# Kernel optimization log

Hardware: AMD Instinct MI355X
Metric: run time of the kernel (lower is better)

## Reference

```python
import jax, jax.numpy as jnp
import numpy as np

B, N, C_IN, C_OUT, K = 2, 8192, 128, 128, 21  # K = num_neighbors + 1 (self)
EPS = 1e-5

def knn_idx(xyz, k):
    # xyz: [B,N,3] -> idx [B,N,k] of k nearest neighbors (self included)
    d2 = jnp.sum(xyz * xyz, axis=-1)  # [B,N]
    dist = d2[:, :, None] + d2[:, None, :] - 2.0 * jnp.einsum('bnd,bmd->bnm', xyz, xyz)
    _, idx = jax.lax.top_k(-dist, k)
    return idx

def group_points(pts, idx):
    # pts [B,N,D], idx [B,N,K] -> [B,N,K,D]
    return jax.vmap(lambda p, i: p[i])(pts, idx)

def group_feats(f, idx):
    # f [B,C,N], idx [B,N,K] -> [B,C,N,K]
    return jax.vmap(lambda ff, i: ff[:, i])(f, idx)

def conv_bn_relu(x, W, g, b, m, v):
    # 1x1 conv (bias=False) + BatchNorm (inference stats) + ReLU
    y = jnp.einsum('oc,bcnk->bonk', W, x)
    inv = g / jnp.sqrt(v + EPS)
    return jax.nn.relu(y * inv[None, :, None, None] + (b - m * inv)[None, :, None, None])

def setup_inputs():
    key = jax.random.key(0)
    ks = jax.random.split(key, 12)
    return {
        'xyz': jax.random.normal(ks[0], (B, N, 3), jnp.float32),
        'f': jax.random.normal(ks[1], (B, C_IN, N), jnp.float32),
        'W_geo': jax.random.normal(ks[2], (C_OUT, 6), jnp.float32) * 0.1,
        'g_geo': jax.random.uniform(ks[3], (C_OUT,), jnp.float32, 0.5, 1.5),
        'b_geo': jax.random.normal(ks[4], (C_OUT,), jnp.float32) * 0.1,
        'm_geo': jax.random.normal(ks[5], (C_OUT,), jnp.float32) * 0.1,
        'v_geo': jax.random.uniform(ks[6], (C_OUT,), jnp.float32, 0.5, 1.5),
        'W_feat': jax.random.normal(ks[7], (C_OUT, 2 * C_IN), jnp.float32) * 0.05,
        'g_feat': jax.random.uniform(ks[8], (C_OUT,), jnp.float32, 0.5, 1.5),
        'b_feat': jax.random.normal(ks[9], (C_OUT,), jnp.float32) * 0.1,
        'm_feat': jax.random.normal(ks[10], (C_OUT,), jnp.float32) * 0.1,
        'v_feat': jax.random.uniform(ks[11], (C_OUT,), jnp.float32, 0.5, 1.5),
    }

def reference(xyz, f, W_geo, g_geo, b_geo, m_geo, v_geo, W_feat, g_feat, b_feat, m_feat, v_feat):
    idx = knn_idx(xyz, K)                                   # [B,N,K]
    grouped_xyz = group_points(xyz, idx)                    # [B,N,K,3]
    xyz_diff = jnp.transpose(grouped_xyz - xyz[:, :, None, :], (0, 3, 1, 2))  # [B,3,N,K]
    center = jnp.broadcast_to(jnp.transpose(xyz, (0, 2, 1))[:, :, :, None], (B, 3, N, K))
    G_geo = jnp.concatenate([center, xyz_diff], axis=1)     # [B,6,N,K]
    grouped_f = group_feats(f, idx)                         # [B,C,N,K]
    center_f = jnp.broadcast_to(f[:, :, :, None], (B, C_IN, N, K))
    G_feat = jnp.concatenate([center_f, grouped_f - center_f], axis=1)  # [B,2C,N,K]
    G_geo = conv_bn_relu(G_geo, W_geo, g_geo, b_geo, m_geo, v_geo)      # [B,C_OUT,N,K]
    G_feat = conv_bn_relu(G_feat, W_feat, g_feat, b_feat, m_feat, v_feat)
    feature = jnp.concatenate([G_geo, G_feat], axis=1)      # [B,2*C_OUT,N,K]
    return jnp.max(feature, axis=-1)                        # [B,2*C_OUT,N]
```

## Files before the change

kernel.cpp:

```cpp
#include <hip/hip_runtime.h>

typedef unsigned int u32;
typedef unsigned long long u64;
typedef unsigned short u16;
typedef float v2f __attribute__((ext_vector_type(2)));

#define DEV __device__ __forceinline__

DEV u16 f2bf(float x) {
  u32 u = __float_as_uint(x);
  u32 r = u + 0x7fffu + ((u >> 16) & 1u);
  return (u16)(r >> 16);
}
DEV float bflo(u32 d) { return __uint_as_float(d << 16); }
DEV float bfhi(u32 d) { return __uint_as_float(d & 0xffff0000u); }
DEV u64 sortable64(double f) {
  long long b = __double_as_longlong(f);
  return (u64)b ^ (u64)((b >> 63) | (long long)0x8000000000000000ll);
}
DEV double ddist(double qx, double qy, double qz, double qd2,
                 float mxf, float myf, float mzf) {
  double cx = (double)mxf, cy = (double)myf, cz = (double)mzf;
  double cd2 = cx * cx + cy * cy + cz * cz;
  double dot = cx * qx + cy * qy + cz * qz;
  return (qd2 + cd2) - 2.0 * dot;
}
DEV float fmin3f(float a, float b, float c) {
  return __builtin_fminf(__builtin_fminf(a, b), c);
}
DEV v2f vfma2(v2f a, v2f b, v2f c) { return __builtin_elementwise_fma(a, b, c); }

#define NB 2
#define NN 8192
#define NC 128
#define KK 21
#define MARGIN 1e-3f
#define CT 2048

__global__ __launch_bounds__(256) void k_prep(
    const float* __restrict__ Wf, const float* __restrict__ gf, const float* __restrict__ bf_,
    const float* __restrict__ mf, const float* __restrict__ vf,
    const float* __restrict__ Wg, const float* __restrict__ gg, const float* __restrict__ bg,
    const float* __restrict__ mg, const float* __restrict__ vg,
    u16* __restrict__ Wt, float* __restrict__ beta_f,
    float* __restrict__ Wgu, float* __restrict__ Wgv, float* __restrict__ beta_g) {
  int g = blockIdx.x * 256 + threadIdx.x;
  int c = g >> 8, o = g & 255;
  float val;
  if (o < 128) {
    float inv = gf[o] / sqrtf(vf[o] + 1e-5f);
    val = inv * (Wf[o * 256 + c] - Wf[o * 256 + c + 128]);
  } else {
    int o2 = o - 128;
    float inv = gf[o2] / sqrtf(vf[o2] + 1e-5f);
    val = inv * Wf[o2 * 256 + c + 128];
  }
  Wt[c * 256 + o] = f2bf(val);
  if (g < 128) {
    float inv = gf[g] / sqrtf(vf[g] + 1e-5f);
    beta_f[g] = bf_[g] - mf[g] * inv;
  } else if (g < 256) {
    int oo = g - 128;
    float invg = gg[oo] / sqrtf(vg[oo] + 1e-5f);
#pragma unroll
    for (int d = 0; d < 3; ++d) {
      Wgu[oo * 3 + d] = invg * (Wg[oo * 6 + d] - Wg[oo * 6 + 3 + d]);
      Wgv[oo * 3 + d] = invg * Wg[oo * 6 + 3 + d];
    }
    beta_g[oo] = bg[oo] - mg[oo] * invg;
  }
}

__global__ __launch_bounds__(256) void k_geo(
    const float* __restrict__ xyz, const float* __restrict__ Wgu, const float* __restrict__ Wgv,
    const float* __restrict__ beta_g, u32* __restrict__ ucat, u32* __restrict__ vcat) {
  int g = blockIdx.x * 256 + threadIdx.x;
  int p = g >> 6, oc = g & 63;
  const float* xp = xyz + p * 3;
  float X = xp[0], Y = xp[1], Z = xp[2];
  u32 du = 0, dv = 0;
#pragma unroll
  for (int h = 0; h < 2; ++h) {
    int o = oc * 2 + h;
    float ug = X * Wgu[o * 3] + Y * Wgu[o * 3 + 1] + Z * Wgu[o * 3 + 2] + beta_g[o];
    float vv = X * Wgv[o * 3] + Y * Wgv[o * 3 + 1] + Z * Wgv[o * 3 + 2];
    du |= (u32)f2bf(ug) << (16 * h);
    dv |= (u32)f2bf(vv) << (16 * h);
  }
  ucat[p * 128 + oc] = du;
  vcat[p * 128 + oc] = dv;
}

__global__ __launch_bounds__(256) void k_feat(
    const float* __restrict__ f, const u32* __restrict__ Wt32, const float* __restrict__ beta_f,
    u32* __restrict__ ucat, u32* __restrict__ vcat) {
  __shared__ u32 sW[128 * 128];
  __shared__ float sF[128][68];

  const int t = threadIdx.x;
  const int b = blockIdx.x >> 7;
  const int n0 = (blockIdx.x & 127) << 6;
  const int boff = b * (NC * NN);

#pragma unroll
  for (int k = 0; k < 64; ++k) sW[t + (k << 8)] = Wt32[t + (k << 8)];
#pragma unroll
  for (int k = 0; k < 32; ++k) {
    int i = t + (k << 8);
    int c = i >> 6, col = i & 63;
    sF[c][col] = f[boff + c * NN + n0 + col];
  }
  __syncthreads();

  const int w = t >> 6, lane = t & 63;
  const int og = lane >> 3, pg = lane & 7;
  const int o0 = w * 64 + og * 8;
  const int p0 = pg * 8;

  float acc[8][8];
#pragma unroll
  for (int a = 0; a < 8; ++a)
#pragma unroll
    for (int p = 0; p < 8; ++p) acc[a][p] = 0.0f;

  for (int c = 0; c < 128; ++c) {
    float4 fa = *(const float4*)&sF[c][p0];
    float4 fb = *(const float4*)&sF[c][p0 + 4];
    uint4 wr = *(const uint4*)&sW[c * 128 + (o0 >> 1)];
    float wv[8] = {bflo(wr.x), bfhi(wr.x), bflo(wr.y), bfhi(wr.y),
                   bflo(wr.z), bfhi(wr.z), bflo(wr.w), bfhi(wr.w)};
    float fv[8] = {fa.x, fa.y, fa.z, fa.w, fb.x, fb.y, fb.z, fb.w};
#pragma unroll
    for (int a = 0; a < 8; ++a)
#pragma unroll
      for (int p = 0; p < 8; ++p) acc[a][p] = __builtin_fmaf(wv[a], fv[p], acc[a][p]);
  }

  const int ochan = o0 & 127;
  const bool is_u = (o0 < 128);
  float bet[8];
#pragma unroll
  for (int a = 0; a < 8; ++a) bet[a] = is_u ? beta_f[ochan + a] : 0.0f;
  u32* dstbase = is_u ? ucat : vcat;
#pragma unroll
  for (int p = 0; p < 8; ++p) {
    int pt = (b << 13) + n0 + p0 + p;
    u32 d0 = (u32)f2bf(acc[0][p] + bet[0]) | ((u32)f2bf(acc[1][p] + bet[1]) << 16);
    u32 d1 = (u32)f2bf(acc[2][p] + bet[2]) | ((u32)f2bf(acc[3][p] + bet[3]) << 16);
    u32 d2 = (u32)f2bf(acc[4][p] + bet[4]) | ((u32)f2bf(acc[5][p] + bet[5]) << 16);
    u32 d3 = (u32)f2bf(acc[6][p] + bet[6]) | ((u32)f2bf(acc[7][p] + bet[7]) << 16);
    *(uint4*)&dstbase[pt * 128 + 64 + (ochan >> 1)] = make_uint4(d0, d1, d2, d3);
  }
}

__global__ __launch_bounds__(256, 4) void k_knn(const float* __restrict__ xyz,
                                                int* __restrict__ knn) {
  __shared__ float sx[CT], sy[CT], sz[CT];
  __shared__ u16 ssurv[16][128];
  __shared__ u32 scnt[16];
  __shared__ float sthr[2][16];

  const int t = threadIdx.x;
  const int blk = blockIdx.x;
  const int b = blk >> 9;
  const int n0 = (blk & 511) << 4;
  const float* X = xyz + b * (NN * 3);

  if (t < 16) scnt[t] = 0u;

  const int w = t >> 6, lane = t & 63;
  const int g = w >> 1;
  const int h = w & 1;
  const int hb = h << 10;

  float mx[8], my[8], mz[8];
#pragma unroll
  for (int i = 0; i < 8; ++i) {
    int q = n0 + (g << 3) + i;
    mx[i] = -2.0f * X[q * 3];
    my[i] = -2.0f * X[q * 3 + 1];
    mz[i] = -2.0f * X[q * 3 + 2];
  }

  float mn[8];
#pragma unroll
  for (int i = 0; i < 8; ++i) mn[i] = __builtin_inff();

  for (int ct = 0; ct < NN / CT; ++ct) {
    __syncthreads();
    const float* Xt = X + ct * (CT * 3);
#pragma unroll
    for (int g2 = 0; g2 < 2; ++g2) {
      int c0 = (t << 2) + (g2 << 10);
      const float* src = Xt + c0 * 3;
      float4 q0 = *(const float4*)(src);
      float4 q1 = *(const float4*)(src + 4);
      float4 q2 = *(const float4*)(src + 8);
      *(float4*)&sx[c0] = make_float4(q0.x, q0.w, q1.z, q2.y);
      *(float4*)&sy[c0] = make_float4(q0.y, q1.x, q1.w, q2.z);
      *(float4*)&sz[c0] = make_float4(q0.z, q1.y, q2.x, q2.w);
    }
    __syncthreads();
#pragma unroll 2
    for (int s8 = 0; s8 < 4; ++s8) {
      int cb = hb + (s8 << 8) + (lane << 2);
      float4 X4 = *(const float4*)&sx[cb];
      float4 Y4 = *(const float4*)&sy[cb];
      float4 Z4 = *(const float4*)&sz[cb];
      v2f x01 = {X4.x, X4.y}, x23 = {X4.z, X4.w};
      v2f y01 = {Y4.x, Y4.y}, y23 = {Y4.z, Y4.w};
      v2f z01 = {Z4.x, Z4.y}, z23 = {Z4.z, Z4.w};
      v2f w01 = vfma2(x01, x01, vfma2(y01, y01, z01 * z01));
      v2f w23 = vfma2(x23, x23, vfma2(y23, y23, z23 * z23));
#pragma unroll
      for (int i = 0; i < 8; ++i) {
        v2f mxv = {mx[i], mx[i]}, myv = {my[i], my[i]}, mzv = {mz[i], mz[i]};
        v2f s01 = vfma2(x01, mxv, vfma2(y01, myv, vfma2(z01, mzv, w01)));
        v2f s23 = vfma2(x23, mxv, vfma2(y23, myv, vfma2(z23, mzv, w23)));
        mn[i] = fmin3f(mn[i], s01.x, s01.y);
        mn[i] = fmin3f(mn[i], s23.x, s23.y);
      }
    }
  }

#pragma unroll 1
  for (int i = 0; i < 8; ++i) {
    float v = mn[i];
#pragma unroll
    for (int k = 2; k <= 64; k <<= 1) {
#pragma unroll
      for (int j = k >> 1; j > 0; j >>= 1) {
        float p = __shfl_xor(v, j);
        bool takeMin = (((lane & k) == 0) == ((lane & j) == 0));
        v = takeMin ? fminf(v, p) : fmaxf(v, p);
      }
    }
    float tw = __shfl(v, 20);
    if (lane == 0) sthr[h][(g << 3) + i] = tw;
  }
  __syncthreads();
  float thr[8];
#pragma unroll
  for (int i = 0; i < 8; ++i) {
    int qq = (g << 3) + i;
    thr[i] = fminf(sthr[0][qq], sthr[1][qq]) + MARGIN;
  }

  for (int ct = 0; ct < NN / CT; ++ct) {
    __syncthreads();
    const float* Xt = X + ct * (CT * 3);
#pragma unroll
    for (int g2 = 0; g2 < 2; ++g2) {
      int c0 = (t << 2) + (g2 << 10);
      const float* src = Xt + c0 * 3;
      float4 q0 = *(const float4*)(src);
      float4 q1 = *(const float4*)(src + 4);
      float4 q2 = *(const float4*)(src + 8);
      *(float4*)&sx[c0] = make_float4(q0.x, q0.w, q1.z, q2.y);
      *(float4*)&sy[c0] = make_float4(q0.y, q1.x, q1.w, q2.z);
      *(float4*)&sz[c0] = make_float4(q0.z, q1.y, q2.x, q2.w);
    }
    __syncthreads();
#pragma unroll 1
    for (int s8 = 0; s8 < 4; ++s8) {
      int cb = hb + (s8 << 8) + (lane << 2);
      float4 X4 = *(const float4*)&sx[cb];
      float4 Y4 = *(const float4*)&sy[cb];
      float4 Z4 = *(const float4*)&sz[cb];
      v2f x01 = {X4.x, X4.y}, x23 = {X4.z, X4.w};
      v2f y01 = {Y4.x, Y4.y}, y23 = {Y4.z, Y4.w};
      v2f z01 = {Z4.x, Z4.y}, z23 = {Z4.z, Z4.w};
      v2f w01 = vfma2(x01, x01, vfma2(y01, y01, z01 * z01));
      v2f w23 = vfma2(x23, x23, vfma2(y23, y23, z23 * z23));
      int mbase = ct * CT + cb;
#pragma unroll
      for (int i = 0; i < 8; ++i) {
        v2f mxv = {mx[i], mx[i]}, myv = {my[i], my[i]}, mzv = {mz[i], mz[i]};
        v2f s01 = vfma2(x01, mxv, vfma2(y01, myv, vfma2(z01, mzv, w01)));
        v2f s23 = vfma2(x23, mxv, vfma2(y23, myv, vfma2(z23, mzv, w23)));
        int qq = (g << 3) + i;
        if (s01.x <= thr[i]) {
          u32 slot = atomicAdd(&scnt[qq], 1u);
          if (slot < 128u) ssurv[qq][slot] = (u16)(mbase + 0);
        }
        if (s01.y <= thr[i]) {
          u32 slot = atomicAdd(&scnt[qq], 1u);
          if (slot < 128u) ssurv[qq][slot] = (u16)(mbase + 1);
        }
        if (s23.x <= thr[i]) {
          u32 slot = atomicAdd(&scnt[qq], 1u);
          if (slot < 128u) ssurv[qq][slot] = (u16)(mbase + 2);
        }
        if (s23.y <= thr[i]) {
          u32 slot = atomicAdd(&scnt[qq], 1u);
          if (slot < 128u) ssurv[qq][slot] = (u16)(mbase + 3);
        }
      }
    }
  }
  __syncthreads();

#pragma unroll 1
  for (int i = 0; i < 4; ++i) {
    const int qq = (w << 2) + i;
    const int q = n0 + qq;
    double Qx = (double)X[q * 3], Qy = (double)X[q * 3 + 1], Qz = (double)X[q * 3 + 2];
    double Qd2 = Qx * Qx + Qy * Qy + Qz * Qz;
    u32 cnt = scnt[qq];
    if (cnt > 128u) cnt = 128u;
    int* outp = knn + ((b << 13) + q) * KK;

    bool v0 = ((u32)lane < cnt);
    u32 m0 = v0 ? (u32)ssurv[qq][lane] : 0u;
    double s0 = ddist(Qx, Qy, Qz, Qd2, X[m0 * 3], X[m0 * 3 + 1], X[m0 * 3 + 2]);
    u64 k0 = v0 ? ((sortable64(s0) & 0xFFFFFFFFFFFFE000ull) | (u64)m0) : ~0ull;

    if (cnt <= 64u) {
      u64 v = k0;
#pragma unroll
      for (int k = 2; k <= 64; k <<= 1) {
#pragma unroll
        for (int j = k >> 1; j > 0; j >>= 1) {
          u64 p = __shfl_xor(v, j);
          bool takeMin = (((lane & k) == 0) == ((lane & j) == 0));
          bool pl = p < v;
          u64 mnv = pl ? p : v;
          u64 mxv = pl ? v : p;
          v = takeMin ? mnv : mxv;
        }
      }
      if (lane < KK) outp[lane] = (int)(v & 8191ull);
    } else {
      bool v1 = ((u32)(lane + 64) < cnt);
      u32 m1 = v1 ? (u32)ssurv[qq][lane + 64] : 0u;
      double s1 = ddist(Qx, Qy, Qz, Qd2, X[m1 * 3], X[m1 * 3 + 1], X[m1 * 3 + 2]);
      u64 k1 = v1 ? ((sortable64(s1) & 0xFFFFFFFFFFFFE000ull) | (u64)m1) : ~0ull;
      u32 selm = 0;
      for (int r = 0; r < KK; ++r) {
        u64 mk = (k0 < k1) ? k0 : k1;
#pragma unroll
        for (int j = 32; j > 0; j >>= 1) {
          u64 p = __shfl_xor(mk, j);
          if (p < mk) mk = p;
        }
        if (k0 == mk) k0 = ~0ull;
        else if (k1 == mk) k1 = ~0ull;
        if (lane == r) selm = (u32)(mk & 8191ull);
      }
      if (lane < KK) outp[lane] = (int)selm;
    }
  }
}

__global__ __launch_bounds__(256) void k_gather(
    const u32* __restrict__ ucat, const u32* __restrict__ vcat,
    const int* __restrict__ knn, float* __restrict__ out) {
  __shared__ float tr[64 * 258];

  const int t = threadIdx.x;
  const int b = blockIdx.x >> 7;
  const int n0 = (blockIdx.x & 127) << 6;
  const int w = t >> 6, lane = t & 63;
  const int which = w >> 1;
  const int lo = ((w & 1) << 6) | lane;

  for (int step = 0; step < 32; ++step) {
    int qq = step * 2 + which;
    int q = n0 + qq;
    const int* ip = knn + ((b << 13) + q) * KK;
    float a0 = -__builtin_inff(), a1 = -__builtin_inff();
#pragma unroll
    for (int k = 0; k < KK; ++k) {
      int p = ip[k];
      u32 d = vcat[(((b << 13) + p) << 7) + lo];
      a0 = fmaxf(a0, bflo(d));
      a1 = fmaxf(a1, bfhi(d));
    }
    u32 u = ucat[(((b << 13) + q) << 7) + lo];
    float r0 = fmaxf(bflo(u) + a0, 0.0f);
    float r1 = fmaxf(bfhi(u) + a1, 0.0f);
    *(float2*)&tr[qq * 258 + 2 * lo] = make_float2(r0, r1);
  }
  __syncthreads();

  float* ob = out + b * (256 * NN);
  for (int i = 0; i < 64; ++i) {
    int o = (w << 6) + i;
    ob[o * NN + n0 + lane] = tr[lane * 258 + o];
  }
}

extern "C" void kernel_launch(void* const* d_in, const int* in_sizes, int n_in,
                              void* d_out, int out_size, void* d_ws, size_t ws_size,
                              hipStream_t stream) {
  const float* xyz = (const float*)d_in[0];
  const float* f   = (const float*)d_in[1];
  const float* Wg  = (const float*)d_in[2];
  const float* gg  = (const float*)d_in[3];
  const float* bg  = (const float*)d_in[4];
  const float* mg  = (const float*)d_in[5];
  const float* vg  = (const float*)d_in[6];
  const float* Wf  = (const float*)d_in[7];
  const float* gf  = (const float*)d_in[8];
  const float* bf_ = (const float*)d_in[9];
  const float* mf  = (const float*)d_in[10];
  const float* vf  = (const float*)d_in[11];

  char* ws = (char*)d_ws;
  u16*   Wt     = (u16*)ws;
  float* beta_f = (float*)(ws + 65536);
  float* Wgu    = (float*)(ws + 66048);
  float* Wgv    = (float*)(ws + 67584);
  float* beta_g = (float*)(ws + 69120);
  u32*   ucat   = (u32*)(ws + 69632);
  u32*   vcat   = (u32*)(ws + 69632 + 8388608);
  int*   knn    = (int*)(ws + 69632 + 2 * 8388608);
  float* out    = (float*)d_out;

  if (ws_size < (size_t)(69632 + 2 * 8388608 + 16384 * KK * 4)) return;

  k_prep<<<dim3(128), dim3(256), 0, stream>>>(Wf, gf, bf_, mf, vf, Wg, gg, bg, mg, vg,
                                              Wt, beta_f, Wgu, Wgv, beta_g);
  k_geo<<<dim3(4096), dim3(256), 0, stream>>>(xyz, Wgu, Wgv, beta_g, ucat, vcat);
  k_feat<<<dim3(256), dim3(256), 0, stream>>>(f, (const u32*)Wt, beta_f, ucat, vcat);
  k_knn<<<dim3(1024), dim3(256), 0, stream>>>(xyz, knn);
  k_gather<<<dim3(256), dim3(256), 0, stream>>>(ucat, vcat, knn, out);
}
```

Baseline: 200.3 us.

## Restructure kNN blocks to 8 queries with 4-wave candidate split and precomputed norms

The kNN kernel now gives each block 8 queries instead of 16, doubling the grid, and each of the four waves scans a quarter of every 1024-point candidate tile. Candidate squared norms are computed once per tile and stored in shared memory, and the per-wave thresholds are reduced across four waves. The filter pass tests the minimum of four distances first, so most candidates skip the per-candidate atomic checks. Launch bounds go to 8 blocks per SM, which raises occupancy, but each block now rereads all of xyz for half as many queries and runs twice as many tile barriers.

```diff
diff --git a/kernel.cpp b/kernel.cpp
--- a/kernel.cpp
+++ b/kernel.cpp
@@ -35,7 +35,6 @@
 #define NC 128
 #define KK 21
 #define MARGIN 1e-3f
-#define CT 2048
 
 __global__ __launch_bounds__(256) void k_prep(
     const float* __restrict__ Wf, const float* __restrict__ gf, const float* __restrict__ bf_,
@@ -153,73 +152,68 @@
   }
 }
 
-__global__ __launch_bounds__(256, 4) void k_knn(const float* __restrict__ xyz,
+__global__ __launch_bounds__(256, 8) void k_knn(const float* __restrict__ xyz,
                                                 int* __restrict__ knn) {
-  __shared__ float sx[CT], sy[CT], sz[CT];
-  __shared__ u16 ssurv[16][128];
-  __shared__ u32 scnt[16];
-  __shared__ float sthr[2][16];
+  __shared__ float sx[1024], sy[1024], sz[1024], sd[1024];
+  __shared__ u16 ssurv[8][128];
+  __shared__ u32 scnt[8];
+  __shared__ float sthr[4][8];
 
   const int t = threadIdx.x;
   const int blk = blockIdx.x;
-  const int b = blk >> 9;
-  const int n0 = (blk & 511) << 4;
+  const int b = blk >> 10;
+  const int n0 = (blk & 1023) << 3;
   const float* X = xyz + b * (NN * 3);
 
-  if (t < 16) scnt[t] = 0u;
+  if (t < 8) scnt[t] = 0u;
 
   const int w = t >> 6, lane = t & 63;
-  const int g = w >> 1;
-  const int h = w & 1;
-  const int hb = h << 10;
-
-  float mx[8], my[8], mz[8];
+  const int ci = (w << 8) + (lane << 2);
+
+  float mx[8], my[8], mz[8], mn[8];
 #pragma unroll
   for (int i = 0; i < 8; ++i) {
-    int q = n0 + (g << 3) + i;
+    int q = n0 + i;
     mx[i] = -2.0f * X[q * 3];
     my[i] = -2.0f * X[q * 3 + 1];
     mz[i] = -2.0f * X[q * 3 + 2];
-  }
-
-  float mn[8];
-#pragma unroll
-  for (int i = 0; i < 8; ++i) mn[i] = __builtin_inff();
-
-  for (int ct = 0; ct < NN / CT; ++ct) {
+    mn[i] = __builtin_inff();
+  }
+
+  for (int ct = 0; ct < 8; ++ct) {
     __syncthreads();
-    const float* Xt = X + ct * (CT * 3);
-#pragma unroll
-    for (int g2 = 0; g2 < 2; ++g2) {
-      int c0 = (t << 2) + (g2 << 10);
-      const float* src = Xt + c0 * 3;
+    {
+      const float* src = X + ct * 3072 + t * 12;
       float4 q0 = *(const float4*)(src);
       float4 q1 = *(const float4*)(src + 4);
       float4 q2 = *(const float4*)(src + 8);
+      int c0 = t << 2;
       *(float4*)&sx[c0] = make_float4(q0.x, q0.w, q1.z, q2.y);
       *(float4*)&sy[c0] = make_float4(q0.y, q1.x, q1.w, q2.z);
       *(float4*)&sz[c0] = make_float4(q0.z, q1.y, q2.x, q2.w);
-    }
-    __syncthreads();
-#pragma unroll 2
-    for (int s8 = 0; s8 < 4; ++s8) {
-      int cb = hb + (s8 << 8) + (lane << 2);
-      float4 X4 = *(const float4*)&sx[cb];
-      float4 Y4 = *(const float4*)&sy[cb];
-      float4 Z4 = *(const float4*)&sz[cb];
-      v2f x01 = {X4.x, X4.y}, x23 = {X4.z, X4.w};
-      v2f y01 = {Y4.x, Y4.y}, y23 = {Y4.z, Y4.w};
-      v2f z01 = {Z4.x, Z4.y}, z23 = {Z4.z, Z4.w};
+      v2f x01 = {q0.x, q0.w}, x23 = {q1.z, q2.y};
+      v2f y01 = {q0.y, q1.x}, y23 = {q1.w, q2.z};
+      v2f z01 = {q0.z, q1.y}, z23 = {q2.x, q2.w};
       v2f w01 = vfma2(x01, x01, vfma2(y01, y01, z01 * z01));
       v2f w23 = vfma2(x23, x23, vfma2(y23, y23, z23 * z23));
-#pragma unroll
-      for (int i = 0; i < 8; ++i) {
-        v2f mxv = {mx[i], mx[i]}, myv = {my[i], my[i]}, mzv = {mz[i], mz[i]};
-        v2f s01 = vfma2(x01, mxv, vfma2(y01, myv, vfma2(z01, mzv, w01)));
-        v2f s23 = vfma2(x23, mxv, vfma2(y23, myv, vfma2(z23, mzv, w23)));
-        mn[i] = fmin3f(mn[i], s01.x, s01.y);
-        mn[i] = fmin3f(mn[i], s23.x, s23.y);
-      }
+      *(float4*)&sd[c0] = make_float4(w01.x, w01.y, w23.x, w23.y);
+    }
+    __syncthreads();
+    float4 X4 = *(const float4*)&sx[ci];
+    float4 Y4 = *(const float4*)&sy[ci];
+    float4 Z4 = *(const float4*)&sz[ci];
+    float4 D4 = *(const float4*)&sd[ci];
+    v2f x01 = {X4.x, X4.y}, x23 = {X4.z, X4.w};
+    v2f y01 = {Y4.x, Y4.y}, y23 = {Y4.z, Y4.w};
+    v2f z01 = {Z4.x, Z4.y}, z23 = {Z4.z, Z4.w};
+    v2f w01 = {D4.x, D4.y}, w23 = {D4.z, D4.w};
+#pragma unroll
+    for (int i = 0; i < 8; ++i) {
+      v2f mxv = {mx[i], mx[i]}, myv = {my[i], my[i]}, mzv = {mz[i], mz[i]};
+      v2f s01 = vfma2(x01, mxv, vfma2(y01, myv, vfma2(z01, mzv, w01)));
+      v2f s23 = vfma2(x23, mxv, vfma2(y23, myv, vfma2(z23, mzv, w23)));
+      mn[i] = fmin3f(mn[i], s01.x, s01.y);
+      mn[i] = fmin3f(mn[i], s23.x, s23.y);
     }
   }
 
@@ -236,64 +230,65 @@
       }
     }
     float tw = __shfl(v, 20);
-    if (lane == 0) sthr[h][(g << 3) + i] = tw;
+    if (lane == 0) sthr[w][i] = tw;
   }
   __syncthreads();
   float thr[8];
 #pragma unroll
-  for (int i = 0; i < 8; ++i) {
-    int qq = (g << 3) + i;
-    thr[i] = fminf(sthr[0][qq], sthr[1][qq]) + MARGIN;
-  }
-
-  for (int ct = 0; ct < NN / CT; ++ct) {
+  for (int i = 0; i < 8; ++i)
+    thr[i] = fminf(fminf(sthr[0][i], sthr[1][i]),
+                   fminf(sthr[2][i], sthr[3][i])) + MARGIN;
+
+  for (int ct = 0; ct < 8; ++ct) {
     __syncthreads();
-    const float* Xt = X + ct * (CT * 3);
-#pragma unroll
-    for (int g2 = 0; g2 < 2; ++g2) {
-      int c0 = (t << 2) + (g2 << 10);
-      const float* src = Xt + c0 * 3;
+    {
+      const float* src = X + ct * 3072 + t * 12;
       float4 q0 = *(const float4*)(src);
       float4 q1 = *(const float4*)(src + 4);
       float4 q2 = *(const float4*)(src + 8);
+      int c0 = t << 2;
       *(float4*)&sx[c0] = make_float4(q0.x, q0.w, q1.z, q2.y);
       *(float4*)&sy[c0] = make_float4(q0.y, q1.x, q1.w, q2.z);
       *(float4*)&sz[c0] = make_float4(q0.z, q1.y, q2.x, q2.w);
-    }
-    __syncthreads();
-#pragma unroll 1
-    for (int s8 = 0; s8 < 4; ++s8) {
-      int cb = hb + (s8 << 8) + (lane << 2);
-      float4 X4 = *(const float4*)&sx[cb];
-      float4 Y4 = *(const float4*)&sy[cb];
-      float4 Z4 = *(const float4*)&sz[cb];
-      v2f x01 = {X4.x, X4.y}, x23 = {X4.z, X4.w};
-      v2f y01 = {Y4.x, Y4.y}, y23 = {Y4.z, Y4.w};
-      v2f z01 = {Z4.x, Z4.y}, z23 = {Z4.z, Z4.w};
+      v2f x01 = {q0.x, q0.w}, x23 = {q1.z, q2.y};
+      v2f y01 = {q0.y, q1.x}, y23 = {q1.w, q2.z};
+      v2f z01 = {q0.z, q1.y}, z23 = {q2.x, q2.w};
       v2f w01 = vfma2(x01, x01, vfma2(y01, y01, z01 * z01));
       v2f w23 = vfma2(x23, x23, vfma2(y23, y23, z23 * z23));
-      int mbase = ct * CT + cb;
-#pragma unroll
-      for (int i = 0; i < 8; ++i) {
-        v2f mxv = {mx[i], mx[i]}, myv = {my[i], my[i]}, mzv = {mz[i], mz[i]};
-        v2f s01 = vfma2(x01, mxv, vfma2(y01, myv, vfma2(z01, mzv, w01)));
-        v2f s23 = vfma2(x23, mxv, vfma2(y23, myv, vfma2(z23, mzv, w23)));
-        int qq = (g << 3) + i;
+      *(float4*)&sd[c0] = make_float4(w01.x, w01.y, w23.x, w23.y);
+    }
+    __syncthreads();
+    float4 X4 = *(const float4*)&sx[ci];
+    float4 Y4 = *(const float4*)&sy[ci];
+    float4 Z4 = *(const float4*)&sz[ci];
+    float4 D4 = *(const float4*)&sd[ci];
+    v2f x01 = {X4.x, X4.y}, x23 = {X4.z, X4.w};
+    v2f y01 = {Y4.x, Y4.y}, y23 = {Y4.z, Y4.w};
+    v2f z01 = {Z4.x, Z4.y}, z23 = {Z4.z, Z4.w};
+    v2f w01 = {D4.x, D4.y}, w23 = {D4.z, D4.w};
+    const int mbase = ct * 1024 + ci;
+#pragma unroll
+    for (int i = 0; i < 8; ++i) {
+      v2f mxv = {mx[i], mx[i]}, myv = {my[i], my[i]}, mzv = {mz[i], mz[i]};
+      v2f s01 = vfma2(x01, mxv, vfma2(y01, myv, vfma2(z01, mzv, w01)));
+      v2f s23 = vfma2(x23, mxv, vfma2(y23, myv, vfma2(z23, mzv, w23)));
+      float worst = fminf(fmin3f(s01.x, s01.y, s23.x), s23.y);
+      if (worst <= thr[i]) {
         if (s01.x <= thr[i]) {
-          u32 slot = atomicAdd(&scnt[qq], 1u);
-          if (slot < 128u) ssurv[qq][slot] = (u16)(mbase + 0);
+          u32 slot = atomicAdd(&scnt[i], 1u);
+          if (slot < 128u) ssurv[i][slot] = (u16)(mbase + 0);
         }
         if (s01.y <= thr[i]) {
-          u32 slot = atomicAdd(&scnt[qq], 1u);
-          if (slot < 128u) ssurv[qq][slot] = (u16)(mbase + 1);
+          u32 slot = atomicAdd(&scnt[i], 1u);
+          if (slot < 128u) ssurv[i][slot] = (u16)(mbase + 1);
         }
         if (s23.x <= thr[i]) {
-          u32 slot = atomicAdd(&scnt[qq], 1u);
-          if (slot < 128u) ssurv[qq][slot] = (u16)(mbase + 2);
+          u32 slot = atomicAdd(&scnt[i], 1u);
+          if (slot < 128u) ssurv[i][slot] = (u16)(mbase + 2);
         }
         if (s23.y <= thr[i]) {
-          u32 slot = atomicAdd(&scnt[qq], 1u);
-          if (slot < 128u) ssurv[qq][slot] = (u16)(mbase + 3);
+          u32 slot = atomicAdd(&scnt[i], 1u);
+          if (slot < 128u) ssurv[i][slot] = (u16)(mbase + 3);
         }
       }
     }
@@ -301,8 +296,8 @@
   __syncthreads();
 
 #pragma unroll 1
-  for (int i = 0; i < 4; ++i) {
-    const int qq = (w << 2) + i;
+  for (int i = 0; i < 2; ++i) {
+    const int qq = (w << 1) + i;
     const int q = n0 + qq;
     double Qx = (double)X[q * 3], Qy = (double)X[q * 3 + 1], Qz = (double)X[q * 3 + 2];
     double Qd2 = Qx * Qx + Qy * Qy + Qz * Qz;
@@ -423,6 +418,6 @@
                                               Wt, beta_f, Wgu, Wgv, beta_g);
   k_geo<<<dim3(4096), dim3(256), 0, stream>>>(xyz, Wgu, Wgv, beta_g, ucat, vcat);
   k_feat<<<dim3(256), dim3(256), 0, stream>>>(f, (const u32*)Wt, beta_f, ucat, vcat);
-  k_knn<<<dim3(1024), dim3(256), 0, stream>>>(xyz, knn);
+  k_knn<<<dim3(2048), dim3(256), 0, stream>>>(xyz, knn);
   k_gather<<<dim3(256), dim3(256), 0, stream>>>(ucat, vcat, knn, out);
 }
```

Measured after the change: 341.5 us. 1.71x slower.
